# Performance work log

Hardware: AMD Instinct MI355X
Metric: run time of the kernel (lower is better)

## Reference

```python
import jax, jax.numpy as jnp
import numpy as np

B, N, D = 2, 8192, 3


def setup_inputs() -> dict:
    key = jax.random.key(0)
    k1, k2, k3 = jax.random.split(key, 3)
    pc1 = jax.random.normal(k1, (B, N, D), dtype=jnp.float32)
    pc2 = jax.random.normal(k2, (B, N, D), dtype=jnp.float32)
    flow = jax.random.normal(k3, (B, N, D), dtype=jnp.float32) * 0.1
    return {"pc1": pc1, "pc2": pc2, "flow": flow}


def reference(pc1, pc2, flow):
    loss_norm = 2
    a = pc1 + flow  # warped pc1, (B, N, 3)
    # pairwise squared distances (B, N, M); argmin of d2 == argmin of true dist
    d2 = (
        jnp.sum(a * a, axis=-1)[:, :, None]
        + jnp.sum(pc2 * pc2, axis=-1)[:, None, :]
        - 2.0 * jnp.einsum("bnd,bmd->bnm", a, pc2)
    )
    # 1-NN of each warped pc1 point in pc2 (idx detached: argmin is non-diff)
    idx1 = jnp.argmin(d2, axis=2)  # (B, N)
    nn1 = jnp.take_along_axis(pc2, idx1[..., None], axis=1)  # (B, N, 3)
    diff1 = a - nn1
    dist1 = jnp.sum(jnp.abs(diff1) ** loss_norm, axis=-1) ** (1.0 / loss_norm)
    # 1-NN of each pc2 point in warped pc1
    idx2 = jnp.argmin(d2, axis=1)  # (B, M)
    nn2 = jnp.take_along_axis(a, idx2[..., None], axis=1)  # (B, M, 3)
    diff2 = pc2 - nn2
    dist2 = jnp.sum(jnp.abs(diff2) ** loss_norm, axis=-1) ** (1.0 / loss_norm)
    return jnp.mean(dist1 + dist2)
```

## Files before the change

### kernel.cpp

```cpp
#include <hip/hip_runtime.h>
#include <math.h>

#define N_PTS   8192
#define BATCH   2
#define NTHR    256
#define QPT     4
#define QPB     (NTHR * QPT)
#define NQB     (N_PTS / QPB)
#define NCHUNK  32
#define CHUNKC  (N_PTS / NCHUNK)
#define TOTQ    (BATCH * 2 * N_PTS)
#define RBLK    (TOTQ / 256)


__global__ __launch_bounds__(256) void chamfer_prep(const float* __restrict__ pc1,
                                                    const float* __restrict__ pc2,
                                                    const float* __restrict__ flow,
                                                    float4* __restrict__ cand,
                                                    unsigned int* __restrict__ minbits,
                                                    float* __restrict__ accum,
                                                    unsigned int* __restrict__ counter) {
    int i = blockIdx.x * 256 + threadIdx.x;
    minbits[i] = 0x7F7FFFFFu;
    if (i < BATCH * N_PTS) {
        float px = pc2[i * 3 + 0], py = pc2[i * 3 + 1], pz = pc2[i * 3 + 2];
        cand[i] = make_float4(-2.f * px, -2.f * py, -2.f * pz,
                              px * px + py * py + pz * pz);
        float wx = pc1[i * 3 + 0] + flow[i * 3 + 0];
        float wy = pc1[i * 3 + 1] + flow[i * 3 + 1];
        float wz = pc1[i * 3 + 2] + flow[i * 3 + 2];
        cand[BATCH * N_PTS + i] = make_float4(-2.f * wx, -2.f * wy, -2.f * wz,
                                              wx * wx + wy * wy + wz * wz);
    }
    if (i == 0) { *accum = 0.0f; *counter = 0u; }
}

__global__ __launch_bounds__(NTHR) void chamfer_nn(const float4* __restrict__ cand,
                                                   unsigned int* __restrict__ minbits) {
    const int qb    = blockIdx.x % NQB;
    const int chunk = blockIdx.x / NQB;
    const int b     = blockIdx.y;
    const int dir   = blockIdx.z;

    const float4* __restrict__ qarr =
        cand + ((size_t)(1 - dir) * BATCH + b) * N_PTS;
    const float4* __restrict__ db =
        cand + ((size_t)dir * BATCH + b) * N_PTS + (size_t)chunk * CHUNKC;

    const int q0 = qb * QPB + threadIdx.x;

    float qx[QPT], qy[QPT], qz[QPT], q2[QPT], m[QPT];
    #pragma unroll
    for (int k = 0; k < QPT; ++k) {
        float4 c = qarr[q0 + k * NTHR];
        qx[k] = -0.5f * c.x;
        qy[k] = -0.5f * c.y;
        qz[k] = -0.5f * c.z;
        q2[k] = c.w;
        m[k]  = 3.402823466e38f;
    }

    #pragma unroll 8
    for (int j = 0; j < CHUNKC; ++j) {
        float4 c = db[j];
        #pragma unroll
        for (int k = 0; k < QPT; ++k) {
            float t = fmaf(qz[k], c.z, c.w);
            t = fmaf(qy[k], c.y, t);
            t = fmaf(qx[k], c.x, t);
            m[k] = fminf(m[k], t);
        }
    }

    unsigned int* __restrict__ slot =
        minbits + ((size_t)dir * BATCH + b) * N_PTS;
    #pragma unroll
    for (int k = 0; k < QPT; ++k) {
        float d2 = fmaxf(m[k] + q2[k], 0.0f);
        atomicMin(&slot[q0 + k * NTHR], __float_as_uint(d2));
    }
}

__global__ __launch_bounds__(256) void chamfer_reduce(const unsigned int* __restrict__ minbits,
                                                      float* __restrict__ accum,
                                                      unsigned int* __restrict__ counter,
                                                      float* __restrict__ out) {
    const int i = blockIdx.x * 256 + threadIdx.x;
    float v = sqrtf(__uint_as_float(minbits[i]));

    for (int off = 32; off > 0; off >>= 1)
        v += __shfl_down(v, off, 64);

    __shared__ float wsum[4];
    const int wave = threadIdx.x >> 6;
    if ((threadIdx.x & 63) == 0) wsum[wave] = v;
    __syncthreads();
    if (threadIdx.x == 0) {
        atomicAdd(accum, wsum[0] + wsum[1] + wsum[2] + wsum[3]);
        __threadfence();
        unsigned int old = atomicAdd(counter, 1u);
        if (old == RBLK - 1) {
            float total = atomicAdd(accum, 0.0f);
            out[0] = total * (1.0f / (float)(BATCH * N_PTS));
        }
    }
}

extern "C" void kernel_launch(void* const* d_in, const int* in_sizes, int n_in,
                              void* d_out, int out_size, void* d_ws, size_t ws_size,
                              hipStream_t stream) {
    const float* pc1  = (const float*)d_in[0];
    const float* pc2  = (const float*)d_in[1];
    const float* flow = (const float*)d_in[2];
    float* out = (float*)d_out;

    float4* cand = (float4*)d_ws;
    unsigned int* minbits = (unsigned int*)(cand + 2 * BATCH * N_PTS);
    float* accum = (float*)(minbits + TOTQ);
    unsigned int* counter = (unsigned int*)(accum + 1);

    chamfer_prep<<<TOTQ / 256, 256, 0, stream>>>(pc1, pc2, flow, cand, minbits,
                                                 accum, counter);

    dim3 grid(NQB * NCHUNK, BATCH, 2);
    chamfer_nn<<<grid, NTHR, 0, stream>>>(cand, minbits);

    chamfer_reduce<<<RBLK, 256, 0, stream>>>(minbits, accum, counter, out);
}
```

Measured before the change: 46.22 us.

## Replace atomicMin merge with per-chunk partial buffers and widen query tiles

Each NN block now writes its per-chunk minimum distances to a dedicated slice of a partial-results buffer instead of doing atomicMin into a shared array. The reduce kernel takes the min over all chunks before the sqrt and sum, so the init store in prep goes away. Queries per thread rise from 4 to 8 and the chunk count from 32 to 64, giving more register reuse of each loaded candidate while keeping the block count the same. The trade-off is a larger workspace and a reduce kernel that reads 64 strided values per query.

```diff
diff --git a/kernel.cpp b/kernel.cpp
--- a/kernel.cpp
+++ b/kernel.cpp
@@ -4,10 +4,10 @@
 #define N_PTS   8192
 #define BATCH   2
 #define NTHR    256
-#define QPT     4
+#define QPT     8
 #define QPB     (NTHR * QPT)
 #define NQB     (N_PTS / QPB)
-#define NCHUNK  32
+#define NCHUNK  64
 #define CHUNKC  (N_PTS / NCHUNK)
 #define TOTQ    (BATCH * 2 * N_PTS)
 #define RBLK    (TOTQ / 256)
@@ -17,11 +17,9 @@
                                                     const float* __restrict__ pc2,
                                                     const float* __restrict__ flow,
                                                     float4* __restrict__ cand,
-                                                    unsigned int* __restrict__ minbits,
                                                     float* __restrict__ accum,
                                                     unsigned int* __restrict__ counter) {
     int i = blockIdx.x * 256 + threadIdx.x;
-    minbits[i] = 0x7F7FFFFFu;
     if (i < BATCH * N_PTS) {
         float px = pc2[i * 3 + 0], py = pc2[i * 3 + 1], pz = pc2[i * 3 + 2];
         cand[i] = make_float4(-2.f * px, -2.f * py, -2.f * pz,
@@ -36,7 +34,7 @@
 }
 
 __global__ __launch_bounds__(NTHR) void chamfer_nn(const float4* __restrict__ cand,
-                                                   unsigned int* __restrict__ minbits) {
+                                                   float* __restrict__ res) {
     const int qb    = blockIdx.x % NQB;
     const int chunk = blockIdx.x / NQB;
     const int b     = blockIdx.y;
@@ -72,21 +70,23 @@
         }
     }
 
-    unsigned int* __restrict__ slot =
-        minbits + ((size_t)dir * BATCH + b) * N_PTS;
+    float* __restrict__ dst =
+        res + (size_t)chunk * TOTQ + ((size_t)dir * BATCH + b) * N_PTS;
     #pragma unroll
-    for (int k = 0; k < QPT; ++k) {
-        float d2 = fmaxf(m[k] + q2[k], 0.0f);
-        atomicMin(&slot[q0 + k * NTHR], __float_as_uint(d2));
-    }
+    for (int k = 0; k < QPT; ++k)
+        dst[q0 + k * NTHR] = fmaxf(m[k] + q2[k], 0.0f);
 }
 
-__global__ __launch_bounds__(256) void chamfer_reduce(const unsigned int* __restrict__ minbits,
+__global__ __launch_bounds__(256) void chamfer_reduce(const float* __restrict__ res,
                                                       float* __restrict__ accum,
                                                       unsigned int* __restrict__ counter,
                                                       float* __restrict__ out) {
     const int i = blockIdx.x * 256 + threadIdx.x;
-    float v = sqrtf(__uint_as_float(minbits[i]));
+    float m = res[i];
+    #pragma unroll 8
+    for (int c = 1; c < NCHUNK; ++c)
+        m = fminf(m, res[(size_t)c * TOTQ + i]);
+    float v = sqrtf(m);
 
     for (int off = 32; off > 0; off >>= 1)
         v += __shfl_down(v, off, 64);
@@ -115,15 +115,15 @@
     float* out = (float*)d_out;
 
     float4* cand = (float4*)d_ws;
-    unsigned int* minbits = (unsigned int*)(cand + 2 * BATCH * N_PTS);
-    float* accum = (float*)(minbits + TOTQ);
+    float*  res  = (float*)(cand + 2 * BATCH * N_PTS);
+    float*  accum = res + (size_t)NCHUNK * TOTQ;
     unsigned int* counter = (unsigned int*)(accum + 1);
 
-    chamfer_prep<<<TOTQ / 256, 256, 0, stream>>>(pc1, pc2, flow, cand, minbits,
-                                                 accum, counter);
+    chamfer_prep<<<(BATCH * N_PTS + 255) / 256, 256, 0, stream>>>(pc1, pc2, flow,
+                                                                  cand, accum, counter);
 
     dim3 grid(NQB * NCHUNK, BATCH, 2);
-    chamfer_nn<<<grid, NTHR, 0, stream>>>(cand, minbits);
+    chamfer_nn<<<grid, NTHR, 0, stream>>>(cand, res);
 
-    chamfer_reduce<<<RBLK, 256, 0, stream>>>(minbits, accum, counter, out);
+    chamfer_reduce<<<RBLK, 256, 0, stream>>>(res, accum, counter, out);
 }
```

New measurement: 56.22 us. 21.6% more time.

## Compute pairwise distances with fp16 MFMA tiles and fuse both NN directions

Applied to the files above, without the earlier changes.

Replaces the scalar FMA nearest-neighbour loop with 16x16x32 fp16 MFMA tiles computing the dot products. A single pass over the distance matrix now yields both the row-wise and column-wise minima, so the matrix is no longer computed twice. Column chunks of pc2 are staged in LDS, and the minima are combined with wave shuffles and atomicMin. Points are quantised to fp16, which may change which neighbour is picked and the resulting distances. Only 3 of the 32 K-slots in each MFMA are non-zero, and column minima need frequent global atomics.

```diff
diff --git a/kernel.cpp b/kernel.cpp
--- a/kernel.cpp
+++ b/kernel.cpp
@@ -3,81 +3,140 @@
 
 #define N_PTS   8192
 #define BATCH   2
-#define NTHR    256
-#define QPT     4
-#define QPB     (NTHR * QPT)
-#define NQB     (N_PTS / QPB)
-#define NCHUNK  32
-#define CHUNKC  (N_PTS / NCHUNK)
-#define TOTQ    (BATCH * 2 * N_PTS)
-#define RBLK    (TOTQ / 256)
+#define WAVES   4
+#define ROWS_PER_WAVE  16
+#define ROWS_PER_BLOCK (WAVES * ROWS_PER_WAVE)
+#define ROW_BLOCKS     (N_PTS / ROWS_PER_BLOCK)
+#define COL_CHUNK      2048
+#define COL_CHUNKS     (N_PTS / COL_CHUNK)
+#define TOTQ (2 * BATCH * N_PTS)
+#define RBLK (TOTQ / 256)
+
+typedef _Float16 half8 __attribute__((ext_vector_type(8)));
+typedef float    f32x4 __attribute__((ext_vector_type(4)));
 
 
 __global__ __launch_bounds__(256) void chamfer_prep(const float* __restrict__ pc1,
                                                     const float* __restrict__ pc2,
                                                     const float* __restrict__ flow,
-                                                    float4* __restrict__ cand,
+                                                    half8* __restrict__ Apk,
+                                                    half8* __restrict__ Bpk,
+                                                    float* __restrict__ q2,
+                                                    float* __restrict__ p2,
                                                     unsigned int* __restrict__ minbits,
                                                     float* __restrict__ accum,
                                                     unsigned int* __restrict__ counter) {
     int i = blockIdx.x * 256 + threadIdx.x;
     minbits[i] = 0x7F7FFFFFu;
     if (i < BATCH * N_PTS) {
-        float px = pc2[i * 3 + 0], py = pc2[i * 3 + 1], pz = pc2[i * 3 + 2];
-        cand[i] = make_float4(-2.f * px, -2.f * py, -2.f * pz,
-                              px * px + py * py + pz * pz);
         float wx = pc1[i * 3 + 0] + flow[i * 3 + 0];
         float wy = pc1[i * 3 + 1] + flow[i * 3 + 1];
         float wz = pc1[i * 3 + 2] + flow[i * 3 + 2];
-        cand[BATCH * N_PTS + i] = make_float4(-2.f * wx, -2.f * wy, -2.f * wz,
-                                              wx * wx + wy * wy + wz * wz);
+        _Float16 hx = (_Float16)wx, hy = (_Float16)wy, hz = (_Float16)wz;
+        float fx = (float)hx, fy = (float)hy, fz = (float)hz;
+        q2[i] = fx * fx + fy * fy + fz * fz;
+        half8 a = {(_Float16)(-0.5f * fx), (_Float16)(-0.5f * fy),
+                   (_Float16)(-0.5f * fz), (_Float16)0.0f,
+                   (_Float16)0.0f, (_Float16)0.0f, (_Float16)0.0f, (_Float16)0.0f};
+        Apk[i] = a;
+
+        float px = pc2[i * 3 + 0], py = pc2[i * 3 + 1], pz = pc2[i * 3 + 2];
+        _Float16 gx = (_Float16)px, gy = (_Float16)py, gz = (_Float16)pz;
+        float ex = (float)gx, ey = (float)gy, ez = (float)gz;
+        p2[i] = ex * ex + ey * ey + ez * ez;
+        half8 bb = {gx, gy, gz, (_Float16)0.0f,
+                    (_Float16)0.0f, (_Float16)0.0f, (_Float16)0.0f, (_Float16)0.0f};
+        Bpk[i] = bb;
     }
     if (i == 0) { *accum = 0.0f; *counter = 0u; }
 }
 
-__global__ __launch_bounds__(NTHR) void chamfer_nn(const float4* __restrict__ cand,
-                                                   unsigned int* __restrict__ minbits) {
-    const int qb    = blockIdx.x % NQB;
-    const int chunk = blockIdx.x / NQB;
-    const int b     = blockIdx.y;
-    const int dir   = blockIdx.z;
+__global__ __launch_bounds__(256, 4) void chamfer_mfma(const half8* __restrict__ Apk,
+                                                       const half8* __restrict__ Bpk,
+                                                       const float* __restrict__ q2,
+                                                       const float* __restrict__ p2,
+                                                       unsigned int* __restrict__ minbits) {
+    __shared__ half8 Blds[COL_CHUNK];
 
-    const float4* __restrict__ qarr =
-        cand + ((size_t)(1 - dir) * BATCH + b) * N_PTS;
-    const float4* __restrict__ db =
-        cand + ((size_t)dir * BATCH + b) * N_PTS + (size_t)chunk * CHUNKC;
+    const int b   = blockIdx.z;
+    const int CC  = blockIdx.x * COL_CHUNK;
+    const int tid = threadIdx.x;
 
-    const int q0 = qb * QPB + threadIdx.x;
+    {
+        const uint4* __restrict__ src = (const uint4*)(Bpk + (size_t)b * N_PTS + CC);
+        uint4* dst = (uint4*)Blds;
+        #pragma unroll
+        for (int k = 0; k < 8; ++k)
+            dst[k * 256 + tid] = src[k * 256 + tid];
+    }
+    __syncthreads();
 
-    float qx[QPT], qy[QPT], qz[QPT], q2[QPT], m[QPT];
+    const int wid  = tid >> 6;
+    const int lane = tid & 63;
+    const int c16  = lane & 15;
+    const int rowbase = blockIdx.y * ROWS_PER_BLOCK + wid * ROWS_PER_WAVE;
+
+    const half8 afrag = Apk[(size_t)b * N_PTS + rowbase + c16];
+    const float q2v   = q2[(size_t)b * N_PTS + rowbase + c16];
+    float q2r[4];
     #pragma unroll
-    for (int k = 0; k < QPT; ++k) {
-        float4 c = qarr[q0 + k * NTHR];
-        qx[k] = -0.5f * c.x;
-        qy[k] = -0.5f * c.y;
-        qz[k] = -0.5f * c.z;
-        q2[k] = c.w;
-        m[k]  = 3.402823466e38f;
-    }
+    for (int r = 0; r < 4; ++r)
+        q2r[r] = __shfl(q2v, (lane >> 4) * 4 + r, 64);
 
-    #pragma unroll 8
-    for (int j = 0; j < CHUNKC; ++j) {
-        float4 c = db[j];
+    const float* __restrict__ p2b = p2 + (size_t)b * N_PTS + CC;
+    unsigned int* __restrict__ colbits =
+        minbits + (size_t)BATCH * N_PTS + (size_t)b * N_PTS;
+    unsigned int* __restrict__ rowbits = minbits + (size_t)b * N_PTS;
+
+    const float INF = 3.402823466e38f;
+    float rm[4] = {INF, INF, INF, INF};
+    float cmin[16];
+    #pragma unroll
+    for (int j = 0; j < 16; ++j) cmin[j] = INF;
+
+    #pragma unroll 1
+    for (int g = 0; g < 8; ++g) {
+        const int tbase = g * 16;
         #pragma unroll
-        for (int k = 0; k < QPT; ++k) {
-            float t = fmaf(qz[k], c.z, c.w);
-            t = fmaf(qy[k], c.y, t);
-            t = fmaf(qx[k], c.x, t);
-            m[k] = fminf(m[k], t);
+        for (int tt = 0; tt < 16; ++tt) {
+            const int t = tbase + tt;
+            const half8 bfrag = Blds[t * 16 + c16];
+            const float p2c   = p2b[t * 16 + c16];
+            f32x4 acc = {0.f, 0.f, 0.f, 0.f};
+            acc = __builtin_amdgcn_mfma_f32_16x16x32_f16(afrag, bfrag, acc, 0, 0, 0);
+            float cl;
+            #pragma unroll
+            for (int r = 0; r < 4; ++r) {
+                float ac = acc[r] + q2r[r];
+                rm[r] = fminf(rm[r], ac + p2c);
+                cl = (r == 0) ? ac : fminf(cl, ac);
+            }
+            cmin[tt] = fminf(cmin[tt], cl + p2c);
+        }
+        #pragma unroll
+        for (int j = 0; j < 16; ++j) {
+            float v = cmin[j];
+            v = fminf(v, __shfl_xor(v, 16, 64));
+            v = fminf(v, __shfl_xor(v, 32, 64));
+            if (lane < 16) {
+                const int col = CC + (tbase + j) * 16 + lane;
+                atomicMin(&colbits[col], __float_as_uint(fmaxf(v, 0.0f)));
+            }
+            cmin[j] = INF;
         }
     }
 
-    unsigned int* __restrict__ slot =
-        minbits + ((size_t)dir * BATCH + b) * N_PTS;
     #pragma unroll
-    for (int k = 0; k < QPT; ++k) {
-        float d2 = fmaxf(m[k] + q2[k], 0.0f);
-        atomicMin(&slot[q0 + k * NTHR], __float_as_uint(d2));
+    for (int r = 0; r < 4; ++r) {
+        float v = rm[r];
+        v = fminf(v, __shfl_xor(v, 1, 64));
+        v = fminf(v, __shfl_xor(v, 2, 64));
+        v = fminf(v, __shfl_xor(v, 4, 64));
+        v = fminf(v, __shfl_xor(v, 8, 64));
+        if ((lane & 15) == 0) {
+            const int row = rowbase + (lane >> 4) * 4 + r;
+            atomicMin(&rowbits[row], __float_as_uint(fmaxf(v, 0.0f)));
+        }
     }
 }
 
@@ -114,16 +173,19 @@
     const float* flow = (const float*)d_in[2];
     float* out = (float*)d_out;
 
-    float4* cand = (float4*)d_ws;
-    unsigned int* minbits = (unsigned int*)(cand + 2 * BATCH * N_PTS);
+    half8* Apk = (half8*)d_ws;
+    half8* Bpk = Apk + BATCH * N_PTS;
+    float* q2  = (float*)(Bpk + BATCH * N_PTS);
+    float* p2  = q2 + BATCH * N_PTS;
+    unsigned int* minbits = (unsigned int*)(p2 + BATCH * N_PTS);
     float* accum = (float*)(minbits + TOTQ);
     unsigned int* counter = (unsigned int*)(accum + 1);
 
-    chamfer_prep<<<TOTQ / 256, 256, 0, stream>>>(pc1, pc2, flow, cand, minbits,
-                                                 accum, counter);
+    chamfer_prep<<<TOTQ / 256, 256, 0, stream>>>(pc1, pc2, flow, Apk, Bpk, q2, p2,
+                                                 minbits, accum, counter);
 
-    dim3 grid(NQB * NCHUNK, BATCH, 2);
-    chamfer_nn<<<grid, NTHR, 0, stream>>>(cand, minbits);
+    dim3 grid(COL_CHUNKS, ROW_BLOCKS, BATCH);
+    chamfer_mfma<<<grid, 256, 0, stream>>>(Apk, Bpk, q2, p2, minbits);
 
     chamfer_reduce<<<RBLK, 256, 0, stream>>>(minbits, accum, counter, out);
 }
```

After: 99.73 us. 2.16x slower.
